# Optimization experiments

Hardware: AMD Instinct MI355X
Metric: run time of the kernel (lower is better)

Reference implementation:

```python
import jax, jax.numpy as jnp
import numpy as np

NUM_HEADS = 16
NUM_UNITS = 1024
NEG = -2.0**32 + 1.0
EPS = 1e-8


def setup_inputs() -> dict:
    key = jax.random.key(0)
    ks = jax.random.split(key, 8)
    B, T, C = 2, 2048, 1024
    U = NUM_UNITS
    x = jax.random.normal(ks[0], (B, T, C), dtype=jnp.float32)
    s = 1.0 / np.sqrt(C)
    Wq = jax.random.normal(ks[1], (C, U), dtype=jnp.float32) * s
    Wk = jax.random.normal(ks[2], (C, U), dtype=jnp.float32) * s
    Wv = jax.random.normal(ks[3], (C, U), dtype=jnp.float32) * s
    bq = jnp.zeros((U,), dtype=jnp.float32)
    bk = jnp.zeros((U,), dtype=jnp.float32)
    bv = jnp.zeros((U,), dtype=jnp.float32)
    gamma = jnp.ones((U,), dtype=jnp.float32)
    beta = jnp.zeros((U,), dtype=jnp.float32)
    return {"x": x, "Wq": Wq, "bq": bq, "Wk": Wk, "bk": bk,
            "Wv": Wv, "bv": bv, "gamma": gamma, "beta": beta}


def _attention(x, Wq, bq, Wk, bk, Wv, bv, gamma, beta):
    B, T, C = x.shape
    H = NUM_HEADS
    U = NUM_UNITS
    dh = U // H
    # Dense projections with relu activation (Keras Dense(activation='relu'))
    Q = jax.nn.relu(x @ Wq + bq)  # [B, T, U]
    K = jax.nn.relu(x @ Wk + bk)
    V = jax.nn.relu(x @ Wv + bv)
    # split into heads: tf.split(axis=2) + concat(axis=0) == [B, T, H, dh]
    Qh = Q.reshape(B, T, H, dh)
    Kh = K.reshape(B, T, H, dh)
    Vh = V.reshape(B, T, H, dh)
    # scaled dot-product scores: scale by sqrt(d_head) (K_ last dim after split)
    scores = jnp.einsum('bqhd,bkhd->bhqk', Qh, Kh) / np.sqrt(dh)
    # key mask: sign(|sum(keys, -1)|) over the ORIGINAL keys input (= x)
    key_mask = jnp.sign(jnp.abs(jnp.sum(x, axis=-1)))  # [B, Tk]
    scores = jnp.where(key_mask[:, None, None, :] == 0, NEG, scores)
    # causal mask (lower-triangular)
    tril = jnp.tril(jnp.ones((T, T), dtype=scores.dtype))
    scores = jnp.where(tril[None, None, :, :] == 0, NEG, scores)
    attn = jax.nn.softmax(scores, axis=-1)
    # query mask: multiply attention rows for zero queries
    query_mask = jnp.sign(jnp.abs(jnp.sum(x, axis=-1)))  # [B, Tq]
    attn = attn * query_mask[:, None, :, None]
    # dropout rate is 0 -> identity
    out = jnp.einsum('bhqk,bkhd->bqhd', attn, Vh).reshape(B, T, U)
    # residual with original queries
    out = out + x
    # layer norm over last axis (tf.nn.moments: biased variance)
    mean = jnp.mean(out, axis=-1, keepdims=True)
    var = jnp.mean((out - mean) ** 2, axis=-1, keepdims=True)
    normalized = (out - mean) / jnp.sqrt(var + EPS)
    return gamma * normalized + beta


def reference(x, Wq, bq, Wk, bk, Wv, bv, gamma, beta):
    return _attention(x, Wq, bq, Wk, bk, Wv, bv, gamma, beta)
```

## Files before the change

kernel.cpp:

```cpp
#include <hip/hip_runtime.h>
#include <math.h>

#define BB 2
#define TT 2048
#define CC 1024
#define UU 1024
#define HH 16
#define DH 64
#define BT (BB*TT)

typedef __attribute__((ext_vector_type(8))) __bf16 bf16x8;
typedef __attribute__((ext_vector_type(4))) __bf16 bf16x4;
typedef __attribute__((ext_vector_type(4))) float f32x4;

#define GLL16(g, l) __builtin_amdgcn_global_load_lds( \
    (__attribute__((address_space(1))) const void*)(g), \
    (__attribute__((address_space(3))) void*)(l), 16, 0, 0)

#define C2EXP 0.18033688011112042f
#define MBIAS 64.0f

__global__ __launch_bounds__(256) void prep_kernel(
    const float* __restrict__ x, float* __restrict__ kadd, __bf16* __restrict__ xb,
    const float* __restrict__ Wq, const float* __restrict__ Wk,
    const float* __restrict__ Wv, __bf16* __restrict__ Wt) {
    const int bx = blockIdx.x;
    const int t = threadIdx.x;
    if (bx < BT) {
        int row = bx;
        float4 v = *(const float4*)&x[(size_t)row * CC + t * 4];
        bf16x4 o;
        o[0] = (__bf16)v.x; o[1] = (__bf16)v.y; o[2] = (__bf16)v.z; o[3] = (__bf16)v.w;
        *(bf16x4*)&xb[(size_t)row * CC + t * 4] = o;
        float s = v.x + v.y + v.z + v.w;
#pragma unroll
        for (int off = 32; off; off >>= 1) s += __shfl_down(s, off, 64);
        __shared__ float red[4];
        int lane = t & 63, w = t >> 6;
        if (lane == 0) red[w] = s;
        __syncthreads();
        if (t == 0) {
            float tot = red[0] + red[1] + red[2] + red[3];
            kadd[row] = (tot == 0.f ? -1.0e30f : 0.f) - MBIAS;
        }
    } else {
        int bz = bx - BT;
        int z = bz >> 8, rem = bz & 255;
        const float* W = z == 0 ? Wq : (z == 1 ? Wk : Wv);
        __bf16* Out = Wt + (size_t)z * CC * UU;
        __shared__ float tile[64][65];
        int n0 = (rem & 15) * 64, k0 = (rem >> 4) * 64;
        int r = t >> 4, c4 = (t & 15) * 4;
#pragma unroll
        for (int i = 0; i < 4; ++i) {
            float4 v = *(const float4*)&W[(size_t)(k0 + r + i * 16) * UU + n0 + c4];
            tile[r + i * 16][c4 + 0] = v.x; tile[r + i * 16][c4 + 1] = v.y;
            tile[r + i * 16][c4 + 2] = v.z; tile[r + i * 16][c4 + 3] = v.w;
        }
        __syncthreads();
#pragma unroll
        for (int i = 0; i < 4; ++i) {
            int nr = r + i * 16;
            bf16x4 o;
            o[0] = (__bf16)tile[c4 + 0][nr]; o[1] = (__bf16)tile[c4 + 1][nr];
            o[2] = (__bf16)tile[c4 + 2][nr]; o[3] = (__bf16)tile[c4 + 3][nr];
            *(bf16x4*)&Out[(size_t)(n0 + nr) * CC + k0 + c4] = o;
        }
    }
}

__global__ __launch_bounds__(256, 4) void qkv_mfma(
    const __bf16* __restrict__ xb, const __bf16* __restrict__ Wt_all,
    const float* __restrict__ bq, const float* __restrict__ bk,
    const float* __restrict__ bv,
    __bf16* __restrict__ Qo, __bf16* __restrict__ Ko, __bf16* __restrict__ VTo) {
    const int z = blockIdx.z;
    const __bf16* Wt = Wt_all + (size_t)z * CC * UU;
    const float* bias = z == 0 ? bq : (z == 1 ? bk : bv);

    const int n0 = blockIdx.x * 128, m0 = blockIdx.y * 128;
    const int t = threadIdx.x, w = t >> 6, lane = t & 63;
    const int quad = lane >> 4, nn = lane & 15;
    const int wr = w >> 1, wc = w & 1;

    __shared__ __bf16 smem[2 * 128 * 64];
    __bf16* As = smem;
    __bf16* Bs = smem + 128 * 64;

    f32x4 acc[4][4];
#pragma unroll
    for (int i = 0; i < 4; ++i)
#pragma unroll
        for (int j = 0; j < 4; ++j) acc[i][j] = (f32x4){0.f, 0.f, 0.f, 0.f};

    for (int k0 = 0; k0 < CC; k0 += 64) {
        __syncthreads();
#pragma unroll
        for (int i = 0; i < 4; ++i) {
            int c = i * 256 + t;
            int row = c >> 3;
            int gc = ((c & 7) ^ (row & 7)) * 8;
            GLL16(&xb[(size_t)(m0 + row) * CC + k0 + gc], &As[c * 8]);
            GLL16(&Wt[(size_t)(n0 + row) * CC + k0 + gc], &Bs[c * 8]);
        }
        __syncthreads();
#pragma unroll
        for (int kk = 0; kk < 2; ++kk) {
            bf16x8 af[4], bfr[4];
#pragma unroll
            for (int i = 0; i < 4; ++i) {
                int R = wr * 64 + i * 16 + nn;
                af[i] = *(const bf16x8*)&As[R * 64 + (((kk * 4 + quad) ^ (R & 7)) * 8)];
            }
#pragma unroll
            for (int j = 0; j < 4; ++j) {
                int R = wc * 64 + j * 16 + nn;
                bfr[j] = *(const bf16x8*)&Bs[R * 64 + (((kk * 4 + quad) ^ (R & 7)) * 8)];
            }
#pragma unroll
            for (int i = 0; i < 4; ++i)
#pragma unroll
                for (int j = 0; j < 4; ++j)
                    acc[i][j] = __builtin_amdgcn_mfma_f32_16x16x32_bf16(af[i], bfr[j], acc[i][j], 0, 0, 0);
        }
    }

    __bf16* cw = &smem[w * 1024];
    float bv4[4];
#pragma unroll
    for (int j = 0; j < 4; ++j) bv4[j] = bias[n0 + wc * 64 + j * 16 + nn];

    if (z < 2) {
        __bf16* Out = z == 0 ? Qo : Ko;
#pragma unroll
        for (int i = 0; i < 4; ++i) {
            __syncthreads();
#pragma unroll
            for (int j = 0; j < 4; ++j)
#pragma unroll
                for (int r = 0; r < 4; ++r)
                    cw[(quad * 4 + r) * 64 + j * 16 + nn] =
                        (__bf16)fmaxf(acc[i][j][r] + bv4[j], 0.f);
            __syncthreads();
            int rr = lane >> 2, cc = (lane & 3) * 16;
            bf16x8 v0 = *(const bf16x8*)&cw[rr * 64 + cc];
            bf16x8 v1 = *(const bf16x8*)&cw[rr * 64 + cc + 8];
            size_t o = (size_t)(m0 + wr * 64 + i * 16 + rr) * UU + n0 + wc * 64 + cc;
            *(bf16x8*)&Out[o] = v0;
            *(bf16x8*)&Out[o + 8] = v1;
        }
    } else {
#pragma unroll
        for (int i = 0; i < 4; ++i) {
            __syncthreads();
#pragma unroll
            for (int j = 0; j < 4; ++j)
#pragma unroll
                for (int r = 0; r < 4; ++r)
                    cw[(j * 16 + nn) * 16 + quad * 4 + r] =
                        (__bf16)fmaxf(acc[i][j][r] + bv4[j], 0.f);
            __syncthreads();
            bf16x8 v0 = *(const bf16x8*)&cw[lane * 16];
            bf16x8 v1 = *(const bf16x8*)&cw[lane * 16 + 8];
            size_t o = (size_t)(n0 + wc * 64 + lane) * BT + m0 + wr * 64 + i * 16;
            *(bf16x8*)&VTo[o] = v0;
            *(bf16x8*)&VTo[o + 8] = v1;
        }
    }
}

__global__ __launch_bounds__(256, 4) void attn_mfma(
    const __bf16* __restrict__ Q, const __bf16* __restrict__ K,
    const __bf16* __restrict__ Vt, const float* __restrict__ kadd,
    __bf16* __restrict__ Obf, float* __restrict__ Op0, float* __restrict__ Op1,
    float* __restrict__ lq0, float* __restrict__ lq1) {
    const int cx = blockIdx.x;
    const int p = cx >> 1, half = cx & 1;
    const int bh = blockIdx.y, b = bh >> 4, h = bh & 15;
    const int col0 = h * 64, rowbase = b * TT;
    const int qa = p, qb = 31 - p;

    const int t = threadIdx.x;
    const int w = t >> 6, lane = t & 63, quad = lane >> 4, nn = lane & 15;
    const int s7 = nn & 7;

    __shared__ __align__(16) __bf16 ks[2][64 * 64];
    __shared__ __align__(16) __bf16 vt[2][64 * 64];
    __shared__ __align__(16) __bf16 ps[64 * 64];

    const int c0 = t;
    const int r0 = c0 >> 3, g0 = ((c0 & 7) ^ (r0 & 7)) * 8;
    const int prow = 16 * w + nn;

    const size_t KSTRIDE = 64 * (size_t)UU;
    const __bf16* kb0 = &K[(size_t)(rowbase + r0) * UU + col0 + g0];
    const __bf16* kb1 = kb0 + 32 * (size_t)UU;
    const __bf16* vb0 = &Vt[(size_t)(col0 + r0) * BT + rowbase + g0];
    const __bf16* vb1 = vb0 + 32 * (size_t)BT;
    const float* kab = &kadd[rowbase + quad * 4];

#define STAGE_TILE(BUF, KP0, KP1, VP0, VP1)   \
    GLL16((KP0), &ks[BUF][c0 * 8]);           \
    GLL16((KP1), &ks[BUF][c0 * 8 + 2048]);    \
    GLL16((VP0), &vt[BUF][c0 * 8]);           \
    GLL16((VP1), &vt[BUF][c0 * 8 + 2048]);

    float lp = 0.f;
    f32x4 oc[4];
#pragma unroll
    for (int dt = 0; dt < 4; ++dt) oc[dt] = (f32x4){0.f, 0.f, 0.f, 0.f};
    int cur = 0;
    f32x4 ka[4];
    bf16x8 bq0, bq1;

#define ATTN_CORE(KSC, VTC, DIAG)                                              \
  {                                                                            \
    const __bf16* ksc = (KSC);                                                 \
    const __bf16* vtc = (VTC);                                                 \
    _Pragma("unroll")                                                          \
    for (int ct = 0; ct < 4; ++ct) {                                           \
      int krow = ct * 16 + nn;                                                 \
      bf16x8 a0 = *(const bf16x8*)&ksc[krow * 64 + ((quad ^ s7) * 8)];         \
      bf16x8 a1 = *(const bf16x8*)&ksc[krow * 64 + (((4 + quad) ^ s7) * 8)];   \
      f32x4 sc = (f32x4){0.f, 0.f, 0.f, 0.f};                                  \
      sc = __builtin_amdgcn_mfma_f32_16x16x32_bf16(a0, bq0, sc, 0, 0, 0);      \
      sc = __builtin_amdgcn_mfma_f32_16x16x32_bf16(a1, bq1, sc, 0, 0, 0);      \
      bf16x4 pw;                                                               \
      _Pragma("unroll")                                                        \
      for (int r = 0; r < 4; ++r) {                                            \
        float arg = fmaf(sc[r], C2EXP, ka[ct][r]);                             \
        if (DIAG) {                                                            \
          int kl = ct * 16 + quad * 4 + r;                                     \
          if (kl > prow) arg = -1.0e30f;                                       \
        }                                                                      \
        float pv = __builtin_amdgcn_exp2f(arg);                                \
        lp += pv;                                                              \
        pw[r] = (__bf16)pv;                                                    \
      }                                                                        \
      int chunk = ct * 2 + (quad >> 1);                                       \
      *(bf16x4*)&ps[prow * 64 + ((chunk ^ s7) * 8) + (quad & 1) * 4] = pw;     \
    }                                                                          \
    bf16x8 bp0 = *(const bf16x8*)&ps[prow * 64 + ((quad ^ s7) * 8)];           \
    bf16x8 bp1 = *(const bf16x8*)&ps[prow * 64 + (((4 + quad) ^ s7) * 8)];     \
    _Pragma("unroll")                                                          \
    for (int dt = 0; dt < 4; ++dt) {                                           \
      int vrow = dt * 16 + nn;                                                 \
      bf16x8 a0 = *(const bf16x8*)&vtc[vrow * 64 + ((quad ^ s7) * 8)];         \
      bf16x8 a1 = *(const bf16x8*)&vtc[vrow * 64 + (((4 + quad) ^ s7) * 8)];   \
      oc[dt] = __builtin_amdgcn_mfma_f32_16x16x32_bf16(a0, bp0, oc[dt], 0, 0, 0); \
      oc[dt] = __builtin_amdgcn_mfma_f32_16x16x32_bf16(a1, bp1, oc[dt], 0, 0, 0); \
    }                                                                          \
  }

    if (half == 0) {
#pragma unroll
        for (int ct = 0; ct < 4; ++ct) ka[ct] = *(const f32x4*)&kab[ct * 16];
        {
            const __bf16* qrow = &Q[(size_t)(rowbase + qa * 64 + prow) * UU + col0];
            bq0 = *(const bf16x8*)&qrow[quad * 8];
            bq1 = *(const bf16x8*)&qrow[32 + quad * 8];
        }
        const __bf16* kp0 = kb0; const __bf16* kp1 = kb1;
        const __bf16* vp0 = vb0; const __bf16* vp1 = vb1;
        STAGE_TILE(0, kp0, kp1, vp0, vp1)
        kp0 += KSTRIDE; kp1 += KSTRIDE; vp0 += 64; vp1 += 64;
        asm volatile("s_waitcnt vmcnt(0)" ::: "memory");
        __builtin_amdgcn_s_barrier();

        for (int kt = 0; kt < qa; ++kt) {
            f32x4 kan[4];
#pragma unroll
            for (int ct = 0; ct < 4; ++ct)
                kan[ct] = *(const f32x4*)&kab[(kt + 1) * 64 + ct * 16];
            STAGE_TILE(cur ^ 1, kp0, kp1, vp0, vp1)
            kp0 += KSTRIDE; kp1 += KSTRIDE; vp0 += 64; vp1 += 64;
            ATTN_CORE(ks[cur], vt[cur], false)
#pragma unroll
            for (int ct = 0; ct < 4; ++ct) ka[ct] = kan[ct];
            cur ^= 1;
            asm volatile("s_waitcnt vmcnt(0)" ::: "memory");
            __builtin_amdgcn_s_barrier();
        }
        {
            f32x4 kan[4];
#pragma unroll
            for (int ct = 0; ct < 4; ++ct) kan[ct] = *(const f32x4*)&kab[ct * 16];
            STAGE_TILE(cur ^ 1, kb0, kb1, vb0, vb1)
            ATTN_CORE(ks[cur], vt[cur], true)
#pragma unroll
            for (int ct = 0; ct < 4; ++ct) ka[ct] = kan[ct];
            cur ^= 1;
            asm volatile("s_waitcnt vmcnt(0)" ::: "memory");
            __builtin_amdgcn_s_barrier();
        }
        {
            float l = lp;
            l += __shfl_xor(l, 16, 64);
            l += __shfl_xor(l, 32, 64);
            const int grow = rowbase + qa * 64 + prow;
            float qsel = (kadd[grow] < -1.0e29f) ? 0.f : 1.f;
            float mult = qsel / fmaxf(l, 1e-37f);
#pragma unroll
            for (int dt = 0; dt < 4; ++dt) {
                bf16x4 ov;
                ov[0] = (__bf16)(oc[dt][0] * mult); ov[1] = (__bf16)(oc[dt][1] * mult);
                ov[2] = (__bf16)(oc[dt][2] * mult); ov[3] = (__bf16)(oc[dt][3] * mult);
                *(bf16x4*)&Obf[(size_t)grow * UU + col0 + dt * 16 + quad * 4] = ov;
            }
        }
        lp = 0.f;
#pragma unroll
        for (int dt = 0; dt < 4; ++dt) oc[dt] = (f32x4){0.f, 0.f, 0.f, 0.f};
        {
            const __bf16* qrow = &Q[(size_t)(rowbase + qb * 64 + prow) * UU + col0];
            bq0 = *(const bf16x8*)&qrow[quad * 8];
            bq1 = *(const bf16x8*)&qrow[32 + quad * 8];
        }
        kp0 = kb0 + KSTRIDE; kp1 = kb1 + KSTRIDE; vp0 = vb0 + 64; vp1 = vb1 + 64;
        const int nb = 16 - p;
        for (int kt = 0; kt < nb - 1; ++kt) {
            f32x4 kan[4];
#pragma unroll
            for (int ct = 0; ct < 4; ++ct)
                kan[ct] = *(const f32x4*)&kab[(kt + 1) * 64 + ct * 16];
            STAGE_TILE(cur ^ 1, kp0, kp1, vp0, vp1)
            kp0 += KSTRIDE; kp1 += KSTRIDE; vp0 += 64; vp1 += 64;
            ATTN_CORE(ks[cur], vt[cur], false)
#pragma unroll
            for (int ct = 0; ct < 4; ++ct) ka[ct] = kan[ct];
            cur ^= 1;
            asm volatile("s_waitcnt vmcnt(0)" ::: "memory");
            __builtin_amdgcn_s_barrier();
        }
        ATTN_CORE(ks[cur], vt[cur], false)
        {
            float l = lp;
            l += __shfl_xor(l, 16, 64);
            l += __shfl_xor(l, 32, 64);
            const int grow = rowbase + qb * 64 + prow;
            if (quad == 0) lq0[(size_t)grow * HH + h] = l;
            size_t orow = (size_t)(grow - (b + 1) * 1024);
#pragma unroll
            for (int dt = 0; dt < 4; ++dt)
                *(f32x4*)&Op0[orow * UU + col0 + dt * 16 + quad * 4] = oc[dt];
        }
    } else {
        const int k0t = 16 - p;
#pragma unroll
        for (int ct = 0; ct < 4; ++ct)
            ka[ct] = *(const f32x4*)&kab[k0t * 64 + ct * 16];
        {
            const __bf16* qrow = &Q[(size_t)(rowbase + qb * 64 + prow) * UU + col0];
            bq0 = *(const bf16x8*)&qrow[quad * 8];
            bq1 = *(const bf16x8*)&qrow[32 + quad * 8];
        }
        const __bf16* kp0 = kb0 + (size_t)k0t * KSTRIDE;
        const __bf16* kp1 = kb1 + (size_t)k0t * KSTRIDE;
        const __bf16* vp0 = vb0 + k0t * 64;
        const __bf16* vp1 = vb1 + k0t * 64;
        STAGE_TILE(0, kp0, kp1, vp0, vp1)
        kp0 += KSTRIDE; kp1 += KSTRIDE; vp0 += 64; vp1 += 64;
        asm volatile("s_waitcnt vmcnt(0)" ::: "memory");
        __builtin_amdgcn_s_barrier();

        for (int i = 0; i < 15; ++i) {
            f32x4 kan[4];
#pragma unroll
            for (int ct = 0; ct < 4; ++ct)
                kan[ct] = *(const f32x4*)&kab[(k0t + i + 1) * 64 + ct * 16];
            STAGE_TILE(cur ^ 1, kp0, kp1, vp0, vp1)
            kp0 += KSTRIDE; kp1 += KSTRIDE; vp0 += 64; vp1 += 64;
            ATTN_CORE(ks[cur], vt[cur], false)
#pragma unroll
            for (int ct = 0; ct < 4; ++ct) ka[ct] = kan[ct];
            cur ^= 1;
            asm volatile("s_waitcnt vmcnt(0)" ::: "memory");
            __builtin_amdgcn_s_barrier();
        }
        ATTN_CORE(ks[cur], vt[cur], true)
        {
            float l = lp;
            l += __shfl_xor(l, 16, 64);
            l += __shfl_xor(l, 32, 64);
            const int grow = rowbase + qb * 64 + prow;
            if (quad == 0) lq1[(size_t)grow * HH + h] = l;
            size_t orow = (size_t)(grow - (b + 1) * 1024);
#pragma unroll
            for (int dt = 0; dt < 4; ++dt)
                *(f32x4*)&Op1[orow * UU + col0 + dt * 16 + quad * 4] = oc[dt];
        }
    }
#undef ATTN_CORE
#undef STAGE_TILE
}

__global__ __launch_bounds__(256) void ln_kernel(
    const __bf16* __restrict__ Obf, const float* __restrict__ Op0,
    const float* __restrict__ Op1, const float* __restrict__ lq0,
    const float* __restrict__ lq1, const float* __restrict__ kadd,
    const float* __restrict__ x, const float* __restrict__ gamma,
    const float* __restrict__ beta, float* __restrict__ out) {
    int row = blockIdx.x;
    int b = row >> 11;
    int qt = (row & (TT - 1)) >> 6;
    size_t base = (size_t)row * UU;
    int t = threadIdx.x;
    float v0, v1, v2, v3;
    float4 xv = *(const float4*)&x[base + t * 4];
    if (qt < 16) {
        bf16x4 ov = *(const bf16x4*)&Obf[base + t * 4];
        v0 = (float)ov[0] + xv.x; v1 = (float)ov[1] + xv.y;
        v2 = (float)ov[2] + xv.z; v3 = (float)ov[3] + xv.w;
    } else {
        int h = t >> 4;
        float l = lq0[(size_t)row * HH + h] + lq1[(size_t)row * HH + h];
        size_t base1 = (size_t)(row - (b + 1) * 1024) * UU;
        f32x4 o0 = *(const f32x4*)&Op0[base1 + t * 4];
        f32x4 o1 = *(const f32x4*)&Op1[base1 + t * 4];
        float qsel = (kadd[row] < -1.0e29f) ? 0.f : 1.f;
        float mult = qsel / fmaxf(l, 1e-37f);
        v0 = (o0[0] + o1[0]) * mult + xv.x; v1 = (o0[1] + o1[1]) * mult + xv.y;
        v2 = (o0[2] + o1[2]) * mult + xv.z; v3 = (o0[3] + o1[3]) * mult + xv.w;
    }
    float s1 = v0 + v1 + v2 + v3;
    float s2 = v0 * v0 + v1 * v1 + v2 * v2 + v3 * v3;
#pragma unroll
    for (int off = 32; off; off >>= 1) {
        s1 += __shfl_down(s1, off, 64);
        s2 += __shfl_down(s2, off, 64);
    }
    __shared__ float r1[4], r2[4];
    int lane = t & 63, w = t >> 6;
    if (lane == 0) { r1[w] = s1; r2[w] = s2; }
    __syncthreads();
    s1 = r1[0] + r1[1] + r1[2] + r1[3];
    s2 = r2[0] + r2[1] + r2[2] + r2[3];
    float mean = s1 * (1.0f / 1024.0f);
    float var = s2 * (1.0f / 1024.0f) - mean * mean;
    float rstd = rsqrtf(var + 1e-8f);
    float4 g = *(const float4*)&gamma[t * 4];
    float4 be = *(const float4*)&beta[t * 4];
    float4 ores;
    ores.x = g.x * (v0 - mean) * rstd + be.x;
    ores.y = g.y * (v1 - mean) * rstd + be.y;
    ores.z = g.z * (v2 - mean) * rstd + be.z;
    ores.w = g.w * (v3 - mean) * rstd + be.w;
    *(float4*)&out[base + t * 4] = ores;
}

extern "C" void kernel_launch(void* const* d_in, const int* in_sizes, int n_in,
                              void* d_out, int out_size, void* d_ws, size_t ws_size,
                              hipStream_t stream) {
    const float* x     = (const float*)d_in[0];
    const float* Wq    = (const float*)d_in[1];
    const float* bq    = (const float*)d_in[2];
    const float* Wk    = (const float*)d_in[3];
    const float* bk    = (const float*)d_in[4];
    const float* Wv    = (const float*)d_in[5];
    const float* bv    = (const float*)d_in[6];
    const float* gamma = (const float*)d_in[7];
    const float* beta  = (const float*)d_in[8];
    float* out = (float*)d_out;

    char* wsb = (char*)d_ws;
    const size_t MB = 1024ull * 1024;
    __bf16* xb  = (__bf16*)(wsb);
    __bf16* Wt  = (__bf16*)(wsb + 8 * MB);
    __bf16* Obf = (__bf16*)(wsb);
    float* Op0  = (float*)(wsb + 8 * MB);
    __bf16* Qb  = (__bf16*)(wsb + 16 * MB);
    __bf16* Kb  = (__bf16*)(wsb + 24 * MB);
    __bf16* Vt  = (__bf16*)(wsb + 32 * MB);
    float* kadd = (float*)(wsb + 40 * MB);
    float* Op1  = (float*)(wsb + 41 * MB);
    float* lq0  = (float*)(wsb + 49 * MB);
    float* lq1  = (float*)(wsb + 50 * MB);

    prep_kernel<<<dim3(BT + 768), dim3(256), 0, stream>>>(x, kadd, xb, Wq, Wk, Wv, Wt);
    qkv_mfma<<<dim3(UU / 128, BT / 128, 3), dim3(256), 0, stream>>>(
        xb, Wt, bq, bk, bv, Qb, Kb, Vt);
    attn_mfma<<<dim3(32, BB * HH), dim3(256), 0, stream>>>(
        Qb, Kb, Vt, kadd, Obf, Op0, Op1, lq0, lq1);
    ln_kernel<<<dim3(BT), dim3(256), 0, stream>>>(
        Obf, Op0, Op1, lq0, lq1, kadd, x, gamma, beta, out);
}
```

Before: 170.9 us.

## Raise MFMA wave priority, fence scheduling, and swap attention grid axes

```diff
diff --git a/kernel.cpp b/kernel.cpp
--- a/kernel.cpp
+++ b/kernel.cpp
@@ -174,9 +174,9 @@
     const __bf16* __restrict__ Vt, const float* __restrict__ kadd,
     __bf16* __restrict__ Obf, float* __restrict__ Op0, float* __restrict__ Op1,
     float* __restrict__ lq0, float* __restrict__ lq1) {
-    const int cx = blockIdx.x;
+    const int bh = blockIdx.x, b = bh >> 4, h = bh & 15;
+    const int cx = blockIdx.y;
     const int p = cx >> 1, half = cx & 1;
-    const int bh = blockIdx.y, b = bh >> 4, h = bh & 15;
     const int col0 = h * 64, rowbase = b * TT;
     const int qa = p, qb = 31 - p;
 
@@ -204,6 +204,11 @@
     GLL16((KP1), &ks[BUF][c0 * 8 + 2048]);    \
     GLL16((VP0), &vt[BUF][c0 * 8]);           \
     GLL16((VP1), &vt[BUF][c0 * 8 + 2048]);
+
+#define LOADKA(KT)                            \
+    _Pragma("unroll")                         \
+    for (int ct = 0; ct < 4; ++ct)            \
+        ka[ct] = *(const f32x4*)&kab[(KT) * 64 + ct * 16];
 
     float lp = 0.f;
     f32x4 oc[4];
@@ -223,8 +228,10 @@
       bf16x8 a0 = *(const bf16x8*)&ksc[krow * 64 + ((quad ^ s7) * 8)];         \
       bf16x8 a1 = *(const bf16x8*)&ksc[krow * 64 + (((4 + quad) ^ s7) * 8)];   \
       f32x4 sc = (f32x4){0.f, 0.f, 0.f, 0.f};                                  \
+      __builtin_amdgcn_s_setprio(1);                                          \
       sc = __builtin_amdgcn_mfma_f32_16x16x32_bf16(a0, bq0, sc, 0, 0, 0);      \
       sc = __builtin_amdgcn_mfma_f32_16x16x32_bf16(a1, bq1, sc, 0, 0, 0);      \
+      __builtin_amdgcn_s_setprio(0);                                          \
       bf16x4 pw;                                                               \
       _Pragma("unroll")                                                        \
       for (int r = 0; r < 4; ++r) {                                            \
@@ -237,11 +244,12 @@
         lp += pv;                                                              \
         pw[r] = (__bf16)pv;                                                    \
       }                                                                        \
-      int chunk = ct * 2 + (quad >> 1);                                       \
+      int chunk = ct * 2 + (quad >> 1);                                        \
       *(bf16x4*)&ps[prow * 64 + ((chunk ^ s7) * 8) + (quad & 1) * 4] = pw;     \
     }                                                                          \
     bf16x8 bp0 = *(const bf16x8*)&ps[prow * 64 + ((quad ^ s7) * 8)];           \
     bf16x8 bp1 = *(const bf16x8*)&ps[prow * 64 + (((4 + quad) ^ s7) * 8)];     \
+    __builtin_amdgcn_s_setprio(1);                                            \
     _Pragma("unroll")                                                          \
     for (int dt = 0; dt < 4; ++dt) {                                           \
       int vrow = dt * 16 + nn;                                                 \
@@ -250,11 +258,10 @@
       oc[dt] = __builtin_amdgcn_mfma_f32_16x16x32_bf16(a0, bp0, oc[dt], 0, 0, 0); \
       oc[dt] = __builtin_amdgcn_mfma_f32_16x16x32_bf16(a1, bp1, oc[dt], 0, 0, 0); \
     }                                                                          \
+    __builtin_amdgcn_s_setprio(0);                                            \
   }
 
     if (half == 0) {
-#pragma unroll
-        for (int ct = 0; ct < 4; ++ct) ka[ct] = *(const f32x4*)&kab[ct * 16];
         {
             const __bf16* qrow = &Q[(size_t)(rowbase + qa * 64 + prow) * UU + col0];
             bq0 = *(const bf16x8*)&qrow[quad * 8];
@@ -268,27 +275,22 @@
         __builtin_amdgcn_s_barrier();
 
         for (int kt = 0; kt < qa; ++kt) {
-            f32x4 kan[4];
-#pragma unroll
-            for (int ct = 0; ct < 4; ++ct)
-                kan[ct] = *(const f32x4*)&kab[(kt + 1) * 64 + ct * 16];
+            LOADKA(kt)
+            __builtin_amdgcn_sched_barrier(0);
             STAGE_TILE(cur ^ 1, kp0, kp1, vp0, vp1)
             kp0 += KSTRIDE; kp1 += KSTRIDE; vp0 += 64; vp1 += 64;
+            __builtin_amdgcn_sched_barrier(0);
             ATTN_CORE(ks[cur], vt[cur], false)
-#pragma unroll
-            for (int ct = 0; ct < 4; ++ct) ka[ct] = kan[ct];
             cur ^= 1;
             asm volatile("s_waitcnt vmcnt(0)" ::: "memory");
             __builtin_amdgcn_s_barrier();
         }
         {
-            f32x4 kan[4];
-#pragma unroll
-            for (int ct = 0; ct < 4; ++ct) kan[ct] = *(const f32x4*)&kab[ct * 16];
+            LOADKA(qa)
+            __builtin_amdgcn_sched_barrier(0);
             STAGE_TILE(cur ^ 1, kb0, kb1, vb0, vb1)
+            __builtin_amdgcn_sched_barrier(0);
             ATTN_CORE(ks[cur], vt[cur], true)
-#pragma unroll
-            for (int ct = 0; ct < 4; ++ct) ka[ct] = kan[ct];
             cur ^= 1;
             asm volatile("s_waitcnt vmcnt(0)" ::: "memory");
             __builtin_amdgcn_s_barrier();
@@ -319,19 +321,17 @@
         kp0 = kb0 + KSTRIDE; kp1 = kb1 + KSTRIDE; vp0 = vb0 + 64; vp1 = vb1 + 64;
         const int nb = 16 - p;
         for (int kt = 0; kt < nb - 1; ++kt) {
-            f32x4 kan[4];
-#pragma unroll
-            for (int ct = 0; ct < 4; ++ct)
-                kan[ct] = *(const f32x4*)&kab[(kt + 1) * 64 + ct * 16];
+            LOADKA(kt)
+            __builtin_amdgcn_sched_barrier(0);
             STAGE_TILE(cur ^ 1, kp0, kp1, vp0, vp1)
             kp0 += KSTRIDE; kp1 += KSTRIDE; vp0 += 64; vp1 += 64;
+            __builtin_amdgcn_sched_barrier(0);
             ATTN_CORE(ks[cur], vt[cur], false)
-#pragma unroll
-            for (int ct = 0; ct < 4; ++ct) ka[ct] = kan[ct];
             cur ^= 1;
             asm volatile("s_waitcnt vmcnt(0)" ::: "memory");
             __builtin_amdgcn_s_barrier();
         }
+        LOADKA(nb - 1)
         ATTN_CORE(ks[cur], vt[cur], false)
         {
             float l = lp;
@@ -346,9 +346,6 @@
         }
     } else {
         const int k0t = 16 - p;
-#pragma unroll
-        for (int ct = 0; ct < 4; ++ct)
-            ka[ct] = *(const f32x4*)&kab[k0t * 64 + ct * 16];
         {
             const __bf16* qrow = &Q[(size_t)(rowbase + qb * 64 + prow) * UU + col0];
             bq0 = *(const bf16x8*)&qrow[quad * 8];
@@ -364,19 +361,17 @@
         __builtin_amdgcn_s_barrier();
 
         for (int i = 0; i < 15; ++i) {
-            f32x4 kan[4];
-#pragma unroll
-            for (int ct = 0; ct < 4; ++ct)
-                kan[ct] = *(const f32x4*)&kab[(k0t + i + 1) * 64 + ct * 16];
+            LOADKA(k0t + i)
+            __builtin_amdgcn_sched_barrier(0);
             STAGE_TILE(cur ^ 1, kp0, kp1, vp0, vp1)
             kp0 += KSTRIDE; kp1 += KSTRIDE; vp0 += 64; vp1 += 64;
+            __builtin_amdgcn_sched_barrier(0);
             ATTN_CORE(ks[cur], vt[cur], false)
-#pragma unroll
-            for (int ct = 0; ct < 4; ++ct) ka[ct] = kan[ct];
             cur ^= 1;
             asm volatile("s_waitcnt vmcnt(0)" ::: "memory");
             __builtin_amdgcn_s_barrier();
         }
+        LOADKA(k0t + 15)
         ATTN_CORE(ks[cur], vt[cur], true)
         {
             float l = lp;
@@ -392,6 +387,7 @@
     }
 #undef ATTN_CORE
 #undef STAGE_TILE
+#undef LOADKA
 }
 
 __global__ __launch_bounds__(256) void ln_kernel(
@@ -479,7 +475,7 @@
     prep_kernel<<<dim3(BT + 768), dim3(256), 0, stream>>>(x, kadd, xb, Wq, Wk, Wv, Wt);
     qkv_mfma<<<dim3(UU / 128, BT / 128, 3), dim3(256), 0, stream>>>(
         xb, Wt, bq, bk, bv, Qb, Kb, Vt);
-    attn_mfma<<<dim3(32, BB * HH), dim3(256), 0, stream>>>(
+    attn_mfma<<<dim3(BB * HH, 32), dim3(256), 0, stream>>>(
         Qb, Kb, Vt, kadd, Obf, Op0, Op1, lq0, lq1);
     ln_kernel<<<dim3(BT), dim3(256), 0, stream>>>(
         Obf, Op0, Op1, lq0, lq1, kadd, x, gamma, beta, out);
```

Result: faster. 167.4 us (-2.0%).
